# Performance work log

Measured on AMD Instinct MI355X. Metric: run time of the kernel, lower is better.

The kernel has to match this reference:

```python
import jax, jax.numpy as jnp
import numpy as np

# Detector / geometry constants (mirrors DRR.__init__ kwargs)
SDD = 1020.0           # source-to-detector distance (mm)
H, W = 160, 160        # detector pixels
DELX, DELY = 2.5, 2.5  # pixel pitch (mm)
X0, Y0 = 0.0, 0.0
VOL = 256              # CT volume is VOL^3 voxels
SPACING = 1.5          # voxel spacing (mm)
EPS = 1e-8


def setup_inputs() -> dict:
    key = jax.random.key(0)
    density = jax.random.uniform(key, (VOL, VOL, VOL), dtype=jnp.float32)
    # rigid camera pose: rotate the C-arm about x; isocenter at the world origin
    th = 0.2
    c, s = np.cos(th), np.sin(th)
    R = np.array([[1, 0, 0], [0, c, -s], [0, s, c]], dtype=np.float32)
    t = R @ np.array([0.0, 0.0, -SDD / 2.0], dtype=np.float32)  # source 510mm from isocenter
    pose = np.eye(4, dtype=np.float32)
    pose[:3, :3], pose[:3, 3] = R, t
    # voxel -> world affine: isotropic spacing, volume centered at the origin
    affine = np.eye(4, dtype=np.float32)
    affine[:3, :3] *= SPACING
    affine[:3, 3] = -SPACING * VOL / 2.0
    affine_inv = jnp.asarray(np.linalg.inv(affine).astype(np.float32))
    return {"density": density, "pose": jnp.asarray(pose)[None], "affine_inv": affine_inv}


def _detector_rays():
    # camera frame: X-ray source at the origin, detector plane at z = SDD
    xs = (jnp.arange(W, dtype=jnp.float32) - (W - 1) / 2.0) * DELX + X0
    ys = (jnp.arange(H, dtype=jnp.float32) - (H - 1) / 2.0) * DELY + Y0
    tx, ty = jnp.meshgrid(xs, ys, indexing="xy")
    targets = jnp.stack([tx.ravel(), ty.ravel(), jnp.full((H * W,), SDD, jnp.float32)], -1)
    source = jnp.zeros((1, 3), jnp.float32)
    return source, targets  # [1,3], [H*W,3]


def _pose_apply(pose, pts):  # pose [B,4,4], pts [N,3] -> [B,N,3]
    return jnp.einsum("bij,nj->bni", pose[:, :3, :3], pts) + pose[:, None, :3, 3]


def _affine_apply(A, pts):  # A [4,4], pts [B,N,3] -> [B,N,3]
    return jnp.einsum("ij,bnj->bni", A[:3, :3], pts) + A[:3, 3]


def _siddon(density, src, tgt, raylen):
    # Exact Siddon line integral. src [B,1,3], tgt [B,N,3] in voxel coords.
    dims = jnp.asarray(density.shape, jnp.float32)
    sd = tgt - src                                   # ray directions [B,N,3]
    sd_safe = jnp.where(jnp.abs(sd) < EPS, EPS, sd)  # avoid div-by-zero
    # parametric entry/exit of the segment with the volume bounding box
    a0 = (0.0 - src) / sd_safe
    a1 = (dims - src) / sd_safe
    amin = jnp.maximum(jnp.max(jnp.minimum(a0, a1), -1), 0.0)  # [B,N]
    amax = jnp.minimum(jnp.min(jnp.maximum(a0, a1), -1), 1.0)
    amax = jnp.maximum(amax, amin)
    # intersections with every axis-aligned voxel plane, sorted per ray
    planes = [
        (jnp.arange(n + 1, dtype=jnp.float32)[None, None, :] - src[..., i:i + 1]) / sd_safe[..., i:i + 1]
        for i, n in enumerate(density.shape)
    ]
    alphas = jnp.sort(jnp.concatenate(planes, -1), -1)          # [B,N,P], P = sum(n_i+1)
    # clamping collapses out-of-volume intersections to zero-length intervals
    alphas = jnp.clip(alphas, amin[..., None], amax[..., None])
    steps = jnp.diff(alphas, axis=-1)                           # [B,N,P-1] segment lengths (in alpha)
    amid = 0.5 * (alphas[..., :-1] + alphas[..., 1:])           # segment midpoints
    # voxel index at each midpoint, computed per axis to avoid a [B,N,P,3] stack
    idx = tuple(
        jnp.clip(jnp.floor(src[..., i:i + 1] + amid * sd[..., i:i + 1]).astype(jnp.int32), 0, density.shape[i] - 1)
        for i in range(3)
    )
    vox = density[idx[0], idx[1], idx[2]]                       # irregular gather [B,N,P-1]
    return jnp.sum(vox * steps, -1) * raylen                    # [B,N]


def reference(density, pose, affine_inv):
    src_c, tgt_c = _detector_rays()
    src_w = _pose_apply(pose, src_c)                 # [B,1,3]
    tgt_w = _pose_apply(pose, tgt_c)                 # [B,N,3]
    raylen = jnp.linalg.norm(tgt_w - src_w, axis=-1)  # img = (target-source).norm(dim=-1)
    src_v = _affine_apply(affine_inv, src_w)          # world -> voxel
    tgt_v = _affine_apply(affine_inv, tgt_w)
    drr = _siddon(density, src_v, tgt_v, raylen)
    return drr.reshape(pose.shape[0], 1, H, W)        # img.view(len(pose), -1, H, W)
```

## Files before the change

### kernel.cpp

```cpp
#include <hip/hip_runtime.h>

static constexpr float F_SDD = 1020.0f;
static constexpr int   DH = 160, DW = 160;
static constexpr float DELX = 2.5f, DELY = 2.5f;
static constexpr int   VOL = 256;
static constexpr int   NRAY = DH * DW;
static constexpr int   TILES_X = DW / 8;
static constexpr int   TILES_Y = DH / 8;
static constexpr int   NTILE = TILES_X * TILES_Y;
static constexpr int   CHUNKS = 8;
static constexpr int   SUBS = 4;
static constexpr int   KB = 4;
static constexpr float EPS = 1e-8f;

extern "C" __global__ void zero_out_kernel(float* __restrict__ out, int n) {
    int i = blockIdx.x * blockDim.x + threadIdx.x;
    if (i < n) out[i] = 0.0f;
}

extern "C" __global__ void __launch_bounds__(256)
drr_siddon_kernel(const float* __restrict__ density,
                  const float* __restrict__ pose,
                  const float* __restrict__ ainv,
                  float* __restrict__ out)
{
    __shared__ float red[256];

    int chunk = blockIdx.x & (CHUNKS - 1);
    int tile  = blockIdx.x >> 3;
    int tx = tile % TILES_X, ty = tile / TILES_X;

    int tid  = threadIdx.x;
    int sub  = tid >> 6;
    int lane = tid & 63;

    int px = tx * 8 + (lane & 7);
    int py = ty * 8 + (lane >> 3);
    int ray = py * DW + px;

    float xs = ((float)px - (DW - 1) * 0.5f) * DELX;
    float ys = ((float)py - (DH - 1) * 0.5f) * DELY;

    float R00 = pose[0], R01 = pose[1], R02 = pose[2],  t0 = pose[3];
    float R10 = pose[4], R11 = pose[5], R12 = pose[6],  t1 = pose[7];
    float R20 = pose[8], R21 = pose[9], R22 = pose[10], t2 = pose[11];

    float sw0 = t0, sw1 = t1, sw2 = t2;
    float tw0 = R00 * xs + R01 * ys + R02 * F_SDD + t0;
    float tw1 = R10 * xs + R11 * ys + R12 * F_SDD + t1;
    float tw2 = R20 * xs + R21 * ys + R22 * F_SDD + t2;

    float dw0 = tw0 - sw0, dw1 = tw1 - sw1, dw2 = tw2 - sw2;
    float raylen = sqrtf(dw0 * dw0 + dw1 * dw1 + dw2 * dw2);

    float A00 = ainv[0], A01 = ainv[1], A02 = ainv[2],  A03 = ainv[3];
    float A10 = ainv[4], A11 = ainv[5], A12 = ainv[6],  A13 = ainv[7];
    float A20 = ainv[8], A21 = ainv[9], A22 = ainv[10], A23 = ainv[11];

    float s0 = A00 * sw0 + A01 * sw1 + A02 * sw2 + A03;
    float s1 = A10 * sw0 + A11 * sw1 + A12 * sw2 + A13;
    float s2 = A20 * sw0 + A21 * sw1 + A22 * sw2 + A23;
    float g0 = A00 * tw0 + A01 * tw1 + A02 * tw2 + A03;
    float g1 = A10 * tw0 + A11 * tw1 + A12 * tw2 + A13;
    float g2 = A20 * tw0 + A21 * tw1 + A22 * tw2 + A23;

    float sd0 = g0 - s0, sd1 = g1 - s1, sd2 = g2 - s2;
    float e0 = (fabsf(sd0) < EPS) ? EPS : sd0;
    float e1 = (fabsf(sd1) < EPS) ? EPS : sd1;
    float e2 = (fabsf(sd2) < EPS) ? EPS : sd2;
    float inv0 = 1.0f / e0, inv1 = 1.0f / e1, inv2 = 1.0f / e2;

    float lo0 = (0.0f - s0) * inv0, hi0 = ((float)VOL - s0) * inv0;
    float lo1 = (0.0f - s1) * inv1, hi1 = ((float)VOL - s1) * inv1;
    float lo2 = (0.0f - s2) * inv2, hi2 = ((float)VOL - s2) * inv2;
    float amin = fmaxf(fmaxf(fminf(lo0, hi0), fminf(lo1, hi1)), fminf(lo2, hi2));
    amin = fmaxf(amin, 0.0f);
    float amax = fminf(fminf(fmaxf(lo0, hi0), fmaxf(lo1, hi1)), fmaxf(lo2, hi2));
    amax = fminf(amax, 1.0f);
    amax = fmaxf(amax, amin);

    float arange  = amax - amin;
    float c_start = amin + arange * ((float)chunk * (1.0f / CHUNKS));
    float c_end   = (chunk == CHUNKS - 1) ? amax
                    : amin + arange * ((float)(chunk + 1) * (1.0f / CHUNKS));
    float crange  = c_end - c_start;
    float a_start = c_start + crange * ((float)sub * (1.0f / SUBS));
    float a_end   = (sub == SUBS - 1) ? c_end
                    : c_start + crange * ((float)(sub + 1) * (1.0f / SUBS));

    float ax0, ax1, ax2, da0, da1, da2;
    if (fabsf(sd0) < EPS) { ax0 = 3.0e38f; da0 = 0.0f; }
    else {
        float p = s0 + a_start * sd0;
        float k = (sd0 > 0.0f) ? (floorf(p) + 1.0f) : (ceilf(p) - 1.0f);
        ax0 = (k - s0) * inv0; da0 = fabsf(inv0);
    }
    if (fabsf(sd1) < EPS) { ax1 = 3.0e38f; da1 = 0.0f; }
    else {
        float p = s1 + a_start * sd1;
        float k = (sd1 > 0.0f) ? (floorf(p) + 1.0f) : (ceilf(p) - 1.0f);
        ax1 = (k - s1) * inv1; da1 = fabsf(inv1);
    }
    if (fabsf(sd2) < EPS) { ax2 = 3.0e38f; da2 = 0.0f; }
    else {
        float p = s2 + a_start * sd2;
        float k = (sd2 > 0.0f) ? (floorf(p) + 1.0f) : (ceilf(p) - 1.0f);
        ax2 = (k - s2) * inv2; da2 = fabsf(inv2);
    }

    float acc = 0.0f;
    float alpha = a_start;
    while (alpha < a_end) {
        float seg[KB];
        float val[KB];
#pragma unroll
        for (int k = 0; k < KB; ++k) {
            float m     = fminf(fminf(ax0, ax1), ax2);
            float astop = fminf(m, a_end);
            float amid  = 0.5f * (alpha + astop);
            seg[k] = fmaxf(astop - alpha, 0.0f);
            int i0 = min(max((int)floorf(s0 + amid * sd0), 0), VOL - 1);
            int i1 = min(max((int)floorf(s1 + amid * sd1), 0), VOL - 1);
            int i2 = min(max((int)floorf(s2 + amid * sd2), 0), VOL - 1);
            val[k] = density[(i0 << 16) | (i1 << 8) | i2];
            if (ax0 <= m) ax0 += da0;
            if (ax1 <= m) ax1 += da1;
            if (ax2 <= m) ax2 += da2;
            alpha = m;
        }
#pragma unroll
        for (int k = 0; k < KB; ++k) acc = fmaf(val[k], seg[k], acc);
    }

    red[tid] = acc;
    __syncthreads();
    if (tid < 64) {
        float total = red[tid] + red[tid + 64] + red[tid + 128] + red[tid + 192];
        atomicAdd(&out[ray], total * raylen);
    }
}

extern "C" void kernel_launch(void* const* d_in, const int* in_sizes, int n_in,
                              void* d_out, int out_size, void* d_ws, size_t ws_size,
                              hipStream_t stream) {
    const float* density = (const float*)d_in[0];
    const float* pose    = (const float*)d_in[1];
    const float* ainv    = (const float*)d_in[2];
    float* out = (float*)d_out;

    hipLaunchKernelGGL(zero_out_kernel, dim3((NRAY + 255) / 256), dim3(256), 0,
                       stream, out, NRAY);

    dim3 block(256);
    dim3 grid(NTILE * CHUNKS);
    hipLaunchKernelGGL(drr_siddon_kernel, grid, block, 0, stream,
                       density, pose, ainv, out);
}
```

Before: 35.57 us.

## Split each ray segment into two interleaved walkers with float4 voxel reuse cache

Each thread now walks its alpha range as two independent halves interleaved in one loop, which exposes two independent dependency chains. Each walker keeps a cached float4 of four consecutive voxels and only reloads when the index leaves that aligned quad, so the many consecutive steps along the fastest axis cost no new load. Index computation is moved to float clamp/trunc/fma. The batched-by-4 load unroll is removed, so memory-level parallelism per walker drops. The data-dependent reload branch may diverge across lanes, and an extra initial split point adds a few extra segments.

```diff
diff --git a/kernel.cpp b/kernel.cpp
--- a/kernel.cpp
+++ b/kernel.cpp
@@ -10,7 +10,6 @@
 static constexpr int   NTILE = TILES_X * TILES_Y;
 static constexpr int   CHUNKS = 8;
 static constexpr int   SUBS = 4;
-static constexpr int   KB = 4;
 static constexpr float EPS = 1e-8f;
 
 extern "C" __global__ void zero_out_kernel(float* __restrict__ out, int n) {
@@ -88,49 +87,65 @@
     float a_end   = (sub == SUBS - 1) ? c_end
                     : c_start + crange * ((float)(sub + 1) * (1.0f / SUBS));
 
-    float ax0, ax1, ax2, da0, da1, da2;
-    if (fabsf(sd0) < EPS) { ax0 = 3.0e38f; da0 = 0.0f; }
-    else {
-        float p = s0 + a_start * sd0;
-        float k = (sd0 > 0.0f) ? (floorf(p) + 1.0f) : (ceilf(p) - 1.0f);
-        ax0 = (k - s0) * inv0; da0 = fabsf(inv0);
-    }
-    if (fabsf(sd1) < EPS) { ax1 = 3.0e38f; da1 = 0.0f; }
-    else {
-        float p = s1 + a_start * sd1;
-        float k = (sd1 > 0.0f) ? (floorf(p) + 1.0f) : (ceilf(p) - 1.0f);
-        ax1 = (k - s1) * inv1; da1 = fabsf(inv1);
-    }
-    if (fabsf(sd2) < EPS) { ax2 = 3.0e38f; da2 = 0.0f; }
-    else {
-        float p = s2 + a_start * sd2;
-        float k = (sd2 > 0.0f) ? (floorf(p) + 1.0f) : (ceilf(p) - 1.0f);
-        ax2 = (k - s2) * inv2; da2 = fabsf(inv2);
+    float a_half = a_start + (a_end - a_start) * 0.5f;
+
+    float da0 = fabsf(inv0), da1 = fabsf(inv1), da2 = fabsf(inv2);
+
+#define AXIS_INIT(a0, ax0, ax1, ax2)                                         \
+    if (fabsf(sd0) < EPS) ax0 = 3.0e38f;                                     \
+    else { float p = s0 + (a0) * sd0;                                        \
+           float kk = (sd0 > 0.0f) ? (floorf(p) + 1.0f) : (ceilf(p) - 1.0f); \
+           ax0 = (kk - s0) * inv0; }                                         \
+    if (fabsf(sd1) < EPS) ax1 = 3.0e38f;                                     \
+    else { float p = s1 + (a0) * sd1;                                        \
+           float kk = (sd1 > 0.0f) ? (floorf(p) + 1.0f) : (ceilf(p) - 1.0f); \
+           ax1 = (kk - s1) * inv1; }                                         \
+    if (fabsf(sd2) < EPS) ax2 = 3.0e38f;                                     \
+    else { float p = s2 + (a0) * sd2;                                        \
+           float kk = (sd2 > 0.0f) ? (floorf(p) + 1.0f) : (ceilf(p) - 1.0f); \
+           ax2 = (kk - s2) * inv2; }
+
+    float axA0, axA1, axA2, axB0, axB1, axB2;
+    AXIS_INIT(a_start, axA0, axA1, axA2)
+    AXIS_INIT(a_half,  axB0, axB1, axB2)
+
+    float alA = a_start, enA = a_half;
+    float alB = a_half,  enB = a_end;
+    float accA = 0.0f, accB = 0.0f;
+    float4 qdA = make_float4(0.f, 0.f, 0.f, 0.f);
+    float4 qdB = make_float4(0.f, 0.f, 0.f, 0.f);
+    int qbA = -8, qbB = -8;
+
+#define STEP(al, en, ax0, ax1, ax2, qb, qd, acc)                             \
+    {                                                                        \
+        float m     = fminf(fminf(ax0, ax1), ax2);                           \
+        float astop = fminf(m, en);                                          \
+        float amid  = 0.5f * (al + astop);                                   \
+        float seg   = fmaxf(astop - al, 0.0f);                               \
+        float c0 = truncf(fminf(fmaxf(fmaf(amid, sd0, s0), 0.0f), 255.0f));  \
+        float c1 = truncf(fminf(fmaxf(fmaf(amid, sd1, s1), 0.0f), 255.0f));  \
+        float c2 = truncf(fminf(fmaxf(fmaf(amid, sd2, s2), 0.0f), 255.0f));  \
+        int idx = (int)fmaf(c0, 65536.0f, fmaf(c1, 256.0f, c2));             \
+        int d = idx - qb;                                                    \
+        if ((unsigned)d >= 4u) {                                             \
+            qb = idx & ~3;                                                   \
+            qd = *(const float4*)(density + qb);                             \
+            d = idx - qb;                                                    \
+        }                                                                    \
+        float v = (d & 2) ? ((d & 1) ? qd.w : qd.z)                          \
+                          : ((d & 1) ? qd.y : qd.x);                         \
+        acc = fmaf(v, seg, acc);                                             \
+        if (ax0 <= m) ax0 += da0;                                            \
+        if (ax1 <= m) ax1 += da1;                                            \
+        if (ax2 <= m) ax2 += da2;                                            \
+        al = m;                                                              \
     }
 
-    float acc = 0.0f;
-    float alpha = a_start;
-    while (alpha < a_end) {
-        float seg[KB];
-        float val[KB];
-#pragma unroll
-        for (int k = 0; k < KB; ++k) {
-            float m     = fminf(fminf(ax0, ax1), ax2);
-            float astop = fminf(m, a_end);
-            float amid  = 0.5f * (alpha + astop);
-            seg[k] = fmaxf(astop - alpha, 0.0f);
-            int i0 = min(max((int)floorf(s0 + amid * sd0), 0), VOL - 1);
-            int i1 = min(max((int)floorf(s1 + amid * sd1), 0), VOL - 1);
-            int i2 = min(max((int)floorf(s2 + amid * sd2), 0), VOL - 1);
-            val[k] = density[(i0 << 16) | (i1 << 8) | i2];
-            if (ax0 <= m) ax0 += da0;
-            if (ax1 <= m) ax1 += da1;
-            if (ax2 <= m) ax2 += da2;
-            alpha = m;
-        }
-#pragma unroll
-        for (int k = 0; k < KB; ++k) acc = fmaf(val[k], seg[k], acc);
+    while ((alA < enA) | (alB < enB)) {
+        STEP(alA, enA, axA0, axA1, axA2, qbA, qdA, accA)
+        STEP(alB, enB, axB0, axB1, axB2, qbB, qdB, accB)
     }
+    float acc = accA + accB;
 
     red[tid] = acc;
     __syncthreads();
```

After: 34.04 us. -4.3%, faster.
